# Kernel optimization log

Hardware: AMD Instinct MI355X
Metric: run time of the kernel (lower is better)

The kernel has to match this reference:

```python
import jax, jax.numpy as jnp
import numpy as np

DIM = 1024
HEADS = 16
HEAD_DIM = DIM // HEADS
FFN = 4096
EPS = 1e-6


def layernorm(x, a, b):
    # torch: mean, std (unbiased, ddof=1), divide by (std + eps)
    mean = jnp.mean(x, axis=-1, keepdims=True)
    std = jnp.std(x, axis=-1, keepdims=True, ddof=1)
    return a * (x - mean) / (std + EPS) + b


def setup_inputs() -> dict:
    key = jax.random.key(0)
    ks = jax.random.split(key, 8)
    B, S = 2, 2048
    x = jax.random.normal(ks[0], (B, S, DIM), dtype=jnp.float32)
    mask = jnp.zeros((1, 1, S, S), dtype=jnp.float32)
    sc = 0.02
    wq = jax.random.normal(ks[1], (DIM, DIM), jnp.float32) * sc
    wk = jax.random.normal(ks[2], (DIM, DIM), jnp.float32) * sc
    wv = jax.random.normal(ks[3], (DIM, DIM), jnp.float32) * sc
    wo = jax.random.normal(ks[4], (DIM, DIM), jnp.float32) * sc
    w1 = jax.random.normal(ks[5], (FFN, DIM), jnp.float32) * sc
    w2 = jax.random.normal(ks[6], (DIM, FFN), jnp.float32) * sc
    a1 = jnp.ones((DIM,), jnp.float32)
    b1 = jnp.zeros((DIM,), jnp.float32)
    a2 = jnp.ones((DIM,), jnp.float32)
    b2 = jnp.zeros((DIM,), jnp.float32)
    return {"x": x, "mask": mask, "wq": wq, "wk": wk, "wv": wv, "wo": wo,
            "w1": w1, "w2": w2, "a1": a1, "b1": b1, "a2": a2, "b2": b2}


def reference(x, mask, wq, wk, wv, wo, w1, w2, a1, b1, a2, b2):
    B, S, _ = x.shape
    # QKV projections (Linear weight is [out, in]; y = x @ W.T)
    q = (x @ wq.T).reshape(B, S, HEADS, HEAD_DIM).transpose(0, 2, 1, 3)
    k = (x @ wk.T).reshape(B, S, HEADS, HEAD_DIM).transpose(0, 2, 1, 3)
    v = (x @ wv.T).reshape(B, S, HEADS, HEAD_DIM).transpose(0, 2, 1, 3)
    scores = jnp.einsum('bhqd,bhkd->bhqk', q, k) / np.sqrt(HEAD_DIM).astype(np.float32)
    scores = scores + mask
    probs = jax.nn.softmax(scores.astype(jnp.float32), axis=-1).astype(q.dtype)
    attn = jnp.einsum('bhqk,bhkd->bhqd', probs, v)
    attn = attn.transpose(0, 2, 1, 3).reshape(B, S, DIM)
    attn_out = attn @ wo.T
    attn_x = layernorm(x + attn_out, a1, b1)
    # FFN with exact (erf) GELU, matching nn.GELU default
    h = jax.nn.gelu(attn_x @ w1.T, approximate=False)
    ffn_out = h @ w2.T
    return layernorm(attn_x + ffn_out, a2, b2)
```

## Files before the change

kernel.cpp:

```cpp
#include <hip/hip_runtime.h>
#include <math.h>

typedef __bf16 bf16x8 __attribute__((ext_vector_type(8)));
typedef float  f32x4  __attribute__((ext_vector_type(4)));
typedef unsigned short us4 __attribute__((ext_vector_type(4)));

__device__ __forceinline__ unsigned short f2bf(float f) {
    union { float f; unsigned int u; } v; v.f = f;
    return (unsigned short)((v.u + 0x7FFFu + ((v.u >> 16) & 1u)) >> 16);
}
__device__ __forceinline__ float bf2f(unsigned short u) {
    union { unsigned int i; float f; } c; c.i = (unsigned)u << 16;
    return c.f;
}
__device__ __forceinline__ unsigned cvt_pk_bf16(float lo, float hi) {
    unsigned r;
    asm("v_cvt_pk_bf16_f32 %0, %1, %2" : "=v"(r) : "v"(lo), "v"(hi));
    return r;
}
__device__ __forceinline__ float exp2_raw(float x) {
    float r;
    asm("v_exp_f32 %0, %1" : "=v"(r) : "v"(x));
    return r;
}
__device__ __forceinline__ void gload_lds16(const unsigned short* g, unsigned short* l) {
    __builtin_amdgcn_global_load_lds((__attribute__((address_space(1))) void*)(g),
                                     (__attribute__((address_space(3))) void*)(l), 16, 0, 0);
}

__global__ __launch_bounds__(256)
void cast_all(const float* __restrict__ x, const float* __restrict__ wq,
              const float* __restrict__ wk, const float* __restrict__ wv,
              const float* __restrict__ wo, const float* __restrict__ w1,
              const float* __restrict__ w2,
              unsigned short* __restrict__ xb, unsigned short* __restrict__ wqkv,
              unsigned short* __restrict__ wob, unsigned short* __restrict__ w1b,
              unsigned short* __restrict__ w2b) {
    const int b = blockIdx.x;
    const float* src; unsigned short* dst; int off;
    if      (b <  4096) { src = x;  dst = xb;             off = b;         }
    else if (b <  5120) { src = wq; dst = wqkv;           off = b - 4096;  }
    else if (b <  6144) { src = wk; dst = wqkv + 1048576; off = b - 5120;  }
    else if (b <  7168) { src = wv; dst = wqkv + 2097152; off = b - 6144;  }
    else if (b <  8192) { src = wo; dst = wob;            off = b - 7168;  }
    else if (b < 12288) { src = w1; dst = w1b;            off = b - 8192;  }
    else                { src = w2; dst = w2b;            off = b - 12288; }
    const int i = off * 1024 + threadIdx.x * 4;
    const float4 v = *reinterpret_cast<const float4*>(src + i);
    us4 o = { f2bf(v.x), f2bf(v.y), f2bf(v.z), f2bf(v.w) };
    *reinterpret_cast<us4*>(dst + i) = o;
}

template<int NBI, int EPI>
__global__ __launch_bounds__(512, 2)
void gemm256(const unsigned short* __restrict__ A, const unsigned short* __restrict__ B,
             void* __restrict__ Cout, int M, int N, int Kstride, int Kc, int NBY) {
    constexpr int BN = NBI * 128;
    constexpr int NI = NBI * 2;
    __shared__ __align__(16) unsigned short Al[3][256 * 32];
    __shared__ __align__(16) unsigned short Bl[3][BN * 32];
    const int tid = threadIdx.x;
    const int l   = tid & 63;
    const int w   = tid >> 6;
    const int wg  = blockIdx.x;
    const int swz = (wg & 7) * (gridDim.x >> 3) + (wg >> 3);
    const int bm  = (swz / NBY) * 256;
    const int bn  = (swz % NBY) * BN;
    const int kbase = blockIdx.y * Kc;
    const int wr  = w >> 2;
    const int wc  = w & 3;
    const int wbase = tid & ~63;

    f32x4 acc[8][NI] = {};

    auto stage = [&](int buf, int kt) {
        const int k0 = kbase + kt * 32;
#pragma unroll
        for (int i = 0; i < 2; ++i) {
            const int ci = i * 512 + tid;
            const int r  = ci >> 2;
            const int cl = (ci & 3) ^ (r & 3) ^ ((r >> 2) & 1);
            gload_lds16(A + (size_t)(bm + r) * Kstride + k0 + cl * 8,
                        &Al[buf][(i * 512 + wbase) * 8]);
        }
#pragma unroll
        for (int i = 0; i < NBI; ++i) {
            const int ci = i * 512 + tid;
            const int r  = ci >> 2;
            const int cl = (ci & 3) ^ (r & 3) ^ ((r >> 2) & 1);
            gload_lds16(B + (size_t)(bn + r) * Kstride + k0 + cl * 8,
                        &Bl[buf][(i * 512 + wbase) * 8]);
        }
    };

    const int nk = Kc >> 5;
    stage(0, 0);
    stage(1, 1);
    asm volatile("s_waitcnt vmcnt(%0)" :: "n"(2 + NBI) : "memory");
    __builtin_amdgcn_s_barrier();

    for (int kt = 0; kt < nk; ++kt) {
        const int cur = kt % 3;
        if (kt + 2 < nk) stage((kt + 2) % 3, kt + 2);
        bf16x8 af[8], bfr[NI];
#pragma unroll
        for (int mi = 0; mi < 8; ++mi) {
            const int r  = wr * 128 + mi * 16 + (l & 15);
            const int cl = (l >> 4) ^ (r & 3) ^ ((r >> 2) & 1);
            af[mi] = *reinterpret_cast<const bf16x8*>(&Al[cur][r * 32 + cl * 8]);
        }
#pragma unroll
        for (int ni = 0; ni < NI; ++ni) {
            const int r  = wc * (NI * 16) + ni * 16 + (l & 15);
            const int cl = (l >> 4) ^ (r & 3) ^ ((r >> 2) & 1);
            bfr[ni] = *reinterpret_cast<const bf16x8*>(&Bl[cur][r * 32 + cl * 8]);
        }
        __builtin_amdgcn_s_setprio(1);
#pragma unroll
        for (int mi = 0; mi < 8; ++mi)
#pragma unroll
            for (int ni = 0; ni < NI; ++ni)
                acc[mi][ni] = __builtin_amdgcn_mfma_f32_16x16x32_bf16(af[mi], bfr[ni], acc[mi][ni], 0, 0, 0);
        __builtin_amdgcn_s_setprio(0);
        if (kt + 1 < nk) {
            if (kt + 2 < nk) {
                asm volatile("s_waitcnt vmcnt(%0)" :: "n"(2 + NBI) : "memory");
            } else {
                asm volatile("s_waitcnt vmcnt(0)" ::: "memory");
            }
            __builtin_amdgcn_s_barrier();
        }
    }

#pragma unroll
    for (int mi = 0; mi < 8; ++mi) {
#pragma unroll
        for (int ni = 0; ni < NI; ++ni) {
#pragma unroll
            for (int rr = 0; rr < 4; ++rr) {
                const int m = bm + wr * 128 + mi * 16 + ((l >> 4) << 2) + rr;
                const int n = bn + wc * (NI * 16) + ni * 16 + (l & 15);
                const float v = acc[mi][ni][rr];
                if (EPI == 1) {
                    unsigned short* C = (unsigned short*)Cout;
                    const int s  = m & 2047;
                    const int bh = ((m >> 11) << 4) | ((n & 1023) >> 6);
                    const int d  = n & 63;
                    if (n < 1024)
                        C[(size_t)(bh * 2048 + s) * 64 + d] = f2bf(v * 0.18033688011112042f);
                    else if (n < 2048)
                        C[(size_t)4194304 + (size_t)(bh * 2048 + s) * 64 + d] = f2bf(v);
                    else
                        C[(size_t)8388608 + ((size_t)bh * 64 + d) * 2048 + s] = f2bf(v);
                } else if (EPI == 2) {
                    const float gl = 0.5f * v * (1.0f + erff(v * 0.70710678118654752f));
                    ((unsigned short*)Cout)[(size_t)m * N + n] = f2bf(gl);
                } else {
                    ((unsigned short*)Cout)[(size_t)blockIdx.y * M * N + (size_t)m * N + n] = f2bf(v);
                }
            }
        }
    }
}

__global__ __launch_bounds__(512, 4)
void attn_kernel(const unsigned short* __restrict__ Q, const unsigned short* __restrict__ Kb,
                 const unsigned short* __restrict__ Vt, unsigned short* __restrict__ out) {
    __shared__ __align__(16) unsigned short kld[2][64 * 64];
    __shared__ __align__(16) unsigned short vld[2][64 * 64];
    __shared__ __align__(16) unsigned short plds[8][16][72];
    const int tid = threadIdx.x;
    const int l   = tid & 63;
    const int w   = tid >> 6;
    const int g   = l >> 4;
    const int q15 = l & 15;
    const int bh  = blockIdx.x & 31;
    const int qt  = blockIdx.x >> 5;
    const int q0  = qt * 128 + w * 16;
    const size_t base = (size_t)bh * 2048 * 64;

    bf16x8 qa0, qa1;
    {
        const unsigned short* qp = Q + base + (size_t)(q0 + q15) * 64 + g * 8;
        qa0 = *reinterpret_cast<const bf16x8*>(qp);
        qa1 = *reinterpret_cast<const bf16x8*>(qp + 32);
    }

    bf16x8 ones;
    {
        us4 o1 = { 0x3F80, 0x3F80, 0x3F80, 0x3F80 };
        bf16x8 t;
        *reinterpret_cast<us4*>(&t) = o1;
        *(reinterpret_cast<us4*>(&t) + 1) = o1;
        ones = t;
    }

    f32x4 oacc[5] = {};
    float mrun = -1e30f;

    auto stage = [&](int buf, int k0) {
        const int r  = tid >> 3;
        const int cs = (tid & 7) ^ (r & 7);
        gload_lds16(Kb + base + (size_t)(k0 + r) * 64 + cs * 8, &kld[buf][(tid & ~63) * 8]);
        gload_lds16(Vt + base + (size_t)r * 2048 + k0 + cs * 8, &vld[buf][(tid & ~63) * 8]);
    };

    stage(0, 0);
    int cur = 0;
    for (int t = 0; t < 32; ++t) {
        __syncthreads();
        if (t + 1 < 32) stage(cur ^ 1, (t + 1) * 64);

        bf16x8 kf[4][2];
#pragma unroll
        for (int ks = 0; ks < 4; ++ks) {
            const int row = ks * 16 + q15;
            const int sw  = row & 7;
            kf[ks][0] = *reinterpret_cast<const bf16x8*>(&kld[cur][row * 64 + ((g    ) ^ sw) * 8]);
            kf[ks][1] = *reinterpret_cast<const bf16x8*>(&kld[cur][row * 64 + ((4 + g) ^ sw) * 8]);
        }
        f32x4 sac[4];
#pragma unroll
        for (int ks = 0; ks < 4; ++ks) {
            f32x4 z = { 0.f, 0.f, 0.f, 0.f };
            z = __builtin_amdgcn_mfma_f32_16x16x32_bf16(kf[ks][0], qa0, z, 0, 0, 0);
            z = __builtin_amdgcn_mfma_f32_16x16x32_bf16(kf[ks][1], qa1, z, 0, 0, 0);
            sac[ks] = z;
        }

        float tm = fmaxf(fmaxf(sac[0][0], sac[0][1]), fmaxf(sac[0][2], sac[0][3]));
#pragma unroll
        for (int ks = 1; ks < 4; ++ks) {
            const float a = fmaxf(sac[ks][0], sac[ks][1]);
            const float b = fmaxf(sac[ks][2], sac[ks][3]);
            tm = fmaxf(tm, fmaxf(a, b));
        }
        tm = fmaxf(tm, __shfl_xor(tm, 16));
        tm = fmaxf(tm, __shfl_xor(tm, 32));
        const bool skip = __all(tm <= mrun + 8.0f);
        const float mnew = skip ? mrun : fmaxf(mrun, tm);
#pragma unroll
        for (int ks = 0; ks < 4; ++ks) {
            const float p0 = exp2_raw(sac[ks][0] - mnew);
            const float p1 = exp2_raw(sac[ks][1] - mnew);
            const float p2 = exp2_raw(sac[ks][2] - mnew);
            const float p3 = exp2_raw(sac[ks][3] - mnew);
            uint2 pk;
            pk.x = cvt_pk_bf16(p0, p1);
            pk.y = cvt_pk_bf16(p2, p3);
            *reinterpret_cast<uint2*>(&plds[w][q15][ks * 16 + g * 4]) = pk;
        }
        if (!skip) {
            const float sc = exp2_raw(mrun - mnew);
            float scr[4];
#pragma unroll
            for (int r = 0; r < 4; ++r) scr[r] = __shfl(sc, (l & 48) | (g * 4 + r));
#pragma unroll
            for (int j = 0; j < 5; ++j)
#pragma unroll
                for (int r = 0; r < 4; ++r) oacc[j][r] *= scr[r];
            mrun = mnew;
        }

        const bf16x8 pa0 = *reinterpret_cast<const bf16x8*>(&plds[w][q15][g * 8]);
        const bf16x8 pa1 = *reinterpret_cast<const bf16x8*>(&plds[w][q15][32 + g * 8]);
#pragma unroll
        for (int j = 0; j < 4; ++j) {
            const int row = j * 16 + q15;
            const int sw  = row & 7;
            const bf16x8 v0 = *reinterpret_cast<const bf16x8*>(&vld[cur][row * 64 + ((g    ) ^ sw) * 8]);
            const bf16x8 v1 = *reinterpret_cast<const bf16x8*>(&vld[cur][row * 64 + ((4 + g) ^ sw) * 8]);
            oacc[j] = __builtin_amdgcn_mfma_f32_16x16x32_bf16(pa0, v0, oacc[j], 0, 0, 0);
            oacc[j] = __builtin_amdgcn_mfma_f32_16x16x32_bf16(pa1, v1, oacc[j], 0, 0, 0);
        }
        oacc[4] = __builtin_amdgcn_mfma_f32_16x16x32_bf16(pa0, ones, oacc[4], 0, 0, 0);
        oacc[4] = __builtin_amdgcn_mfma_f32_16x16x32_bf16(pa1, ones, oacc[4], 0, 0, 0);
        cur ^= 1;
    }

    const int b = bh >> 4, h = bh & 15;
#pragma unroll
    for (int r = 0; r < 4; ++r) {
        const float inv = 1.f / oacc[4][r];
        const int q = q0 + g * 4 + r;
#pragma unroll
        for (int j = 0; j < 4; ++j)
            out[(size_t)(b * 2048 + q) * 1024 + h * 64 + j * 16 + q15] = f2bf(oacc[j][r] * inv);
    }
}

template<int NP>
__global__ __launch_bounds__(256)
void ln_res(const float* __restrict__ X, const unsigned short* __restrict__ P,
            const float* __restrict__ gamma, const float* __restrict__ beta,
            float* __restrict__ o32, unsigned short* __restrict__ o16) {
    __shared__ float red[4];
    const int t = threadIdx.x;
    const size_t row = blockIdx.x;
    const float4 a = *reinterpret_cast<const float4*>(X + row * 1024 + t * 4);
    float v0 = a.x, v1 = a.y, v2 = a.z, v3 = a.w;
#pragma unroll
    for (int p = 0; p < NP; ++p) {
        const us4 rr = *reinterpret_cast<const us4*>(P + (size_t)p * 4194304 + row * 1024 + t * 4);
        v0 += bf2f(rr.x); v1 += bf2f(rr.y); v2 += bf2f(rr.z); v3 += bf2f(rr.w);
    }
    float s = v0 + v1 + v2 + v3;
#pragma unroll
    for (int o = 1; o < 64; o <<= 1) s += __shfl_xor(s, o);
    if ((t & 63) == 0) red[t >> 6] = s;
    __syncthreads();
    const float mean = (red[0] + red[1] + red[2] + red[3]) * (1.f / 1024.f);
    v0 -= mean; v1 -= mean; v2 -= mean; v3 -= mean;
    float q = v0 * v0 + v1 * v1 + v2 * v2 + v3 * v3;
#pragma unroll
    for (int o = 1; o < 64; o <<= 1) q += __shfl_xor(q, o);
    __syncthreads();
    if ((t & 63) == 0) red[t >> 6] = q;
    __syncthreads();
    const float var = (red[0] + red[1] + red[2] + red[3]) * (1.f / 1023.f);
    const float inv = 1.f / (sqrtf(var) + 1e-6f);
    const float4 g  = *reinterpret_cast<const float4*>(gamma + t * 4);
    const float4 be = *reinterpret_cast<const float4*>(beta + t * 4);
    const float y0 = g.x * v0 * inv + be.x;
    const float y1 = g.y * v1 * inv + be.y;
    const float y2 = g.z * v2 * inv + be.z;
    const float y3 = g.w * v3 * inv + be.w;
    float4 o4; o4.x = y0; o4.y = y1; o4.z = y2; o4.w = y3;
    *reinterpret_cast<float4*>(o32 + row * 1024 + t * 4) = o4;
    if (o16) {
        us4 ob = { f2bf(y0), f2bf(y1), f2bf(y2), f2bf(y3) };
        *reinterpret_cast<us4*>(o16 + row * 1024 + t * 4) = ob;
    }
}

extern "C" void kernel_launch(void* const* d_in, const int* in_sizes, int n_in,
                              void* d_out, int out_size, void* d_ws, size_t ws_size,
                              hipStream_t stream) {
    const float* x  = (const float*)d_in[0];
    const float* wq = (const float*)d_in[2];
    const float* wk = (const float*)d_in[3];
    const float* wv = (const float*)d_in[4];
    const float* wo = (const float*)d_in[5];
    const float* w1 = (const float*)d_in[6];
    const float* w2 = (const float*)d_in[7];
    const float* a1 = (const float*)d_in[8];
    const float* b1 = (const float*)d_in[9];
    const float* a2 = (const float*)d_in[10];
    const float* b2 = (const float*)d_in[11];

    char* ws = (char*)d_ws;
    const size_t MB = 1024 * 1024;
    unsigned short* xb      = (unsigned short*)(ws);
    unsigned short* wqkv    = (unsigned short*)(ws + 8  * MB);
    unsigned short* wob     = (unsigned short*)(ws + 14 * MB);
    unsigned short* hbuf    = (unsigned short*)(ws);
    unsigned short* w1b     = (unsigned short*)(ws + 32 * MB);
    unsigned short* w2b     = (unsigned short*)(ws + 40 * MB);
    unsigned short* qkv     = (unsigned short*)(ws + 48 * MB);
    unsigned short* projp   = (unsigned short*)(ws + 48 * MB);
    unsigned short* ffn2p   = (unsigned short*)(ws + 48 * MB);
    unsigned short* attn    = (unsigned short*)(ws + 80 * MB);
    float*          attn_x  = (float*)(ws + 88 * MB);
    unsigned short* attn_xb = (unsigned short*)(ws + 104 * MB);

    cast_all<<<16384, 256, 0, stream>>>(x, wq, wk, wv, wo, w1, w2, xb, wqkv, wob, w1b, w2b);
    gemm256<1, 1><<<dim3(384, 1), 512, 0, stream>>>(xb, wqkv, qkv, 4096, 3072, 1024, 1024, 24);
    attn_kernel<<<512, 512, 0, stream>>>(qkv, qkv + 4194304, qkv + 8388608, attn);
    gemm256<2, 3><<<dim3(64, 4), 512, 0, stream>>>(attn, wob, projp, 4096, 1024, 1024, 256, 4);
    ln_res<4><<<4096, 256, 0, stream>>>(x, projp, a1, b1, attn_x, attn_xb);
    gemm256<2, 2><<<dim3(256, 1), 512, 0, stream>>>(attn_xb, w1b, hbuf, 4096, 4096, 1024, 1024, 16);
    gemm256<2, 3><<<dim3(64, 4), 512, 0, stream>>>(hbuf, w2b, ffn2p, 4096, 1024, 4096, 1024, 4);
    ln_res<4><<<4096, 256, 0, stream>>>(attn_x, ffn2p, a2, b2, (float*)d_out, nullptr);
}
```

Before: 271.9 us.

## Replace triple-buffered K=32 GEMM with double-buffered K=64 two-phase 256x256 GEMM

The GEMM kernel now uses a fixed 256x256 output tile with a K-step of 64, double-buffered in LDS, and runs two MFMA phases per stage. It replaces the earlier triple-buffered K=32 pipeline with variable tile width. The LDS layout uses a new XOR swizzle over 8 chunks, and a single __syncthreads per 64-wide K step replaces the fine-grained vmcnt waits. This halves the barrier count and gives each tile more reuse. The QKV GEMM grid drops to 192 blocks, which leaves fewer blocks than CUs. LDS use also grows to 128KB per block, which may lower occupancy and weaken load/compute overlap.

```diff
diff --git a/kernel.cpp b/kernel.cpp
--- a/kernel.cpp
+++ b/kernel.cpp
@@ -51,95 +51,104 @@
     *reinterpret_cast<us4*>(dst + i) = o;
 }
 
-template<int NBI, int EPI>
+template<int EPI>
 __global__ __launch_bounds__(512, 2)
-void gemm256(const unsigned short* __restrict__ A, const unsigned short* __restrict__ B,
-             void* __restrict__ Cout, int M, int N, int Kstride, int Kc, int NBY) {
-    constexpr int BN = NBI * 128;
-    constexpr int NI = NBI * 2;
-    __shared__ __align__(16) unsigned short Al[3][256 * 32];
-    __shared__ __align__(16) unsigned short Bl[3][BN * 32];
+void gemm2ph(const unsigned short* __restrict__ A, const unsigned short* __restrict__ B,
+             void* __restrict__ Cout, int M, int N, int Ks, int Kc, int NBY) {
+    __shared__ __align__(16) unsigned short Al[2][256 * 64];
+    __shared__ __align__(16) unsigned short Bl[2][256 * 64];
     const int tid = threadIdx.x;
     const int l   = tid & 63;
     const int w   = tid >> 6;
+    const int q15 = l & 15;
+    const int g   = l >> 4;
+    const int wr  = w >> 2;
+    const int wc  = w & 3;
     const int wg  = blockIdx.x;
     const int swz = (wg & 7) * (gridDim.x >> 3) + (wg >> 3);
     const int bm  = (swz / NBY) * 256;
-    const int bn  = (swz % NBY) * BN;
+    const int bn  = (swz % NBY) * 256;
     const int kbase = blockIdx.y * Kc;
-    const int wr  = w >> 2;
-    const int wc  = w & 3;
-    const int wbase = tid & ~63;
-
-    f32x4 acc[8][NI] = {};
-
-    auto stage = [&](int buf, int kt) {
-        const int k0 = kbase + kt * 32;
-#pragma unroll
-        for (int i = 0; i < 2; ++i) {
-            const int ci = i * 512 + tid;
-            const int r  = ci >> 2;
-            const int cl = (ci & 3) ^ (r & 3) ^ ((r >> 2) & 1);
-            gload_lds16(A + (size_t)(bm + r) * Kstride + k0 + cl * 8,
-                        &Al[buf][(i * 512 + wbase) * 8]);
-        }
-#pragma unroll
-        for (int i = 0; i < NBI; ++i) {
-            const int ci = i * 512 + tid;
-            const int r  = ci >> 2;
-            const int cl = (ci & 3) ^ (r & 3) ^ ((r >> 2) & 1);
-            gload_lds16(B + (size_t)(bn + r) * Kstride + k0 + cl * 8,
-                        &Bl[buf][(i * 512 + wbase) * 8]);
-        }
+    const int NT  = Kc >> 6;
+
+    const int gta = wc * 64 + l;
+    const int hb  = wc >> 1;
+    const int gtb = (wr * 2 + (wc & 1)) * 64 + l;
+    const int csa = (gta & 7) ^ ((gta >> 3) & 7);
+    const int csb = (gtb & 7) ^ ((gtb >> 3) & 7);
+    const unsigned short* aS = A + (size_t)(bm + wr * 128 + (gta >> 3)) * Ks + kbase + csa * 8;
+    const unsigned short* bS = B + (size_t)(bn + hb * 128 + (gtb >> 3)) * Ks + kbase + csb * 8;
+    const int adst = wr * 8192 + wc * 512;
+    const int bdst = hb * 8192 + (wr * 2 + (wc & 1)) * 512;
+
+    auto stgA = [&](int buf, int j, int ko) {
+        gload_lds16(aS + (size_t)j * 32 * Ks + ko, &Al[0][0] + buf * 16384 + adst + j * 2048);
     };
-
-    const int nk = Kc >> 5;
-    stage(0, 0);
-    stage(1, 1);
-    asm volatile("s_waitcnt vmcnt(%0)" :: "n"(2 + NBI) : "memory");
-    __builtin_amdgcn_s_barrier();
-
-    for (int kt = 0; kt < nk; ++kt) {
-        const int cur = kt % 3;
-        if (kt + 2 < nk) stage((kt + 2) % 3, kt + 2);
-        bf16x8 af[8], bfr[NI];
-#pragma unroll
-        for (int mi = 0; mi < 8; ++mi) {
-            const int r  = wr * 128 + mi * 16 + (l & 15);
-            const int cl = (l >> 4) ^ (r & 3) ^ ((r >> 2) & 1);
-            af[mi] = *reinterpret_cast<const bf16x8*>(&Al[cur][r * 32 + cl * 8]);
-        }
-#pragma unroll
-        for (int ni = 0; ni < NI; ++ni) {
-            const int r  = wc * (NI * 16) + ni * 16 + (l & 15);
-            const int cl = (l >> 4) ^ (r & 3) ^ ((r >> 2) & 1);
-            bfr[ni] = *reinterpret_cast<const bf16x8*>(&Bl[cur][r * 32 + cl * 8]);
-        }
-        __builtin_amdgcn_s_setprio(1);
-#pragma unroll
-        for (int mi = 0; mi < 8; ++mi)
-#pragma unroll
-            for (int ni = 0; ni < NI; ++ni)
-                acc[mi][ni] = __builtin_amdgcn_mfma_f32_16x16x32_bf16(af[mi], bfr[ni], acc[mi][ni], 0, 0, 0);
-        __builtin_amdgcn_s_setprio(0);
-        if (kt + 1 < nk) {
-            if (kt + 2 < nk) {
-                asm volatile("s_waitcnt vmcnt(%0)" :: "n"(2 + NBI) : "memory");
-            } else {
-                asm volatile("s_waitcnt vmcnt(0)" ::: "memory");
-            }
-            __builtin_amdgcn_s_barrier();
-        }
+    auto stgB = [&](int buf, int j, int ko) {
+        gload_lds16(bS + (size_t)j * 32 * Ks + ko, &Bl[0][0] + buf * 16384 + bdst + j * 2048);
+    };
+
+    const int xk0 = g ^ (q15 & 7);
+    const int xk1 = xk0 ^ 4;
+    const int aRd = (wr * 128 + q15) * 64;
+    const int bRd = (hb * 128 + (wc & 1) * 64 + q15) * 64;
+
+    f32x4 acc[8][4] = {};
+
+#pragma unroll
+    for (int j = 0; j < 4; ++j) { stgA(0, j, 0); stgB(0, j, 0); }
+    __syncthreads();
+
+    for (int T = 0; T < NT; ++T) {
+        const int cur = T & 1, nxt = cur ^ 1;
+        const int ko  = (T + 1) << 6;
+        if (T + 1 < NT) {
+#pragma unroll
+            for (int j = 0; j < 4; ++j) { stgA(nxt, j, ko); stgB(nxt, j, ko); }
+        }
+        {
+            bf16x8 a[8], b[4];
+#pragma unroll
+            for (int mi = 0; mi < 8; ++mi)
+                a[mi] = *reinterpret_cast<const bf16x8*>(&Al[0][0] + cur * 16384 + aRd + mi * 1024 + xk0 * 8);
+#pragma unroll
+            for (int ni = 0; ni < 4; ++ni)
+                b[ni] = *reinterpret_cast<const bf16x8*>(&Bl[0][0] + cur * 16384 + bRd + ni * 1024 + xk0 * 8);
+            __builtin_amdgcn_s_setprio(1);
+#pragma unroll
+            for (int mi = 0; mi < 8; ++mi)
+#pragma unroll
+                for (int ni = 0; ni < 4; ++ni)
+                    acc[mi][ni] = __builtin_amdgcn_mfma_f32_16x16x32_bf16(a[mi], b[ni], acc[mi][ni], 0, 0, 0);
+            __builtin_amdgcn_s_setprio(0);
+        }
+        {
+            bf16x8 a[8], b[4];
+#pragma unroll
+            for (int mi = 0; mi < 8; ++mi)
+                a[mi] = *reinterpret_cast<const bf16x8*>(&Al[0][0] + cur * 16384 + aRd + mi * 1024 + xk1 * 8);
+#pragma unroll
+            for (int ni = 0; ni < 4; ++ni)
+                b[ni] = *reinterpret_cast<const bf16x8*>(&Bl[0][0] + cur * 16384 + bRd + ni * 1024 + xk1 * 8);
+            __builtin_amdgcn_s_setprio(1);
+#pragma unroll
+            for (int mi = 0; mi < 8; ++mi)
+#pragma unroll
+                for (int ni = 0; ni < 4; ++ni)
+                    acc[mi][ni] = __builtin_amdgcn_mfma_f32_16x16x32_bf16(a[mi], b[ni], acc[mi][ni], 0, 0, 0);
+            __builtin_amdgcn_s_setprio(0);
+        }
+        __syncthreads();
     }
 
 #pragma unroll
     for (int mi = 0; mi < 8; ++mi) {
 #pragma unroll
-        for (int ni = 0; ni < NI; ++ni) {
+        for (int ni = 0; ni < 4; ++ni) {
 #pragma unroll
             for (int rr = 0; rr < 4; ++rr) {
-                const int m = bm + wr * 128 + mi * 16 + ((l >> 4) << 2) + rr;
-                const int n = bn + wc * (NI * 16) + ni * 16 + (l & 15);
+                const int m = bm + wr * 128 + mi * 16 + (g << 2) + rr;
+                const int n = bn + wc * 64 + ni * 16 + q15;
                 const float v = acc[mi][ni][rr];
                 if (EPI == 1) {
                     unsigned short* C = (unsigned short*)Cout;
@@ -364,11 +373,11 @@
     unsigned short* attn_xb = (unsigned short*)(ws + 104 * MB);
 
     cast_all<<<16384, 256, 0, stream>>>(x, wq, wk, wv, wo, w1, w2, xb, wqkv, wob, w1b, w2b);
-    gemm256<1, 1><<<dim3(384, 1), 512, 0, stream>>>(xb, wqkv, qkv, 4096, 3072, 1024, 1024, 24);
+    gemm2ph<1><<<dim3(192, 1), 512, 0, stream>>>(xb, wqkv, qkv, 4096, 3072, 1024, 1024, 12);
     attn_kernel<<<512, 512, 0, stream>>>(qkv, qkv + 4194304, qkv + 8388608, attn);
-    gemm256<2, 3><<<dim3(64, 4), 512, 0, stream>>>(attn, wob, projp, 4096, 1024, 1024, 256, 4);
+    gemm2ph<3><<<dim3(64, 4), 512, 0, stream>>>(attn, wob, projp, 4096, 1024, 1024, 256, 4);
     ln_res<4><<<4096, 256, 0, stream>>>(x, projp, a1, b1, attn_x, attn_xb);
-    gemm256<2, 2><<<dim3(256, 1), 512, 0, stream>>>(attn_xb, w1b, hbuf, 4096, 4096, 1024, 1024, 16);
-    gemm256<2, 3><<<dim3(64, 4), 512, 0, stream>>>(hbuf, w2b, ffn2p, 4096, 1024, 4096, 1024, 4);
+    gemm2ph<2><<<dim3(256, 1), 512, 0, stream>>>(attn_xb, w1b, hbuf, 4096, 4096, 1024, 1024, 16);
+    gemm2ph<3><<<dim3(64, 4), 512, 0, stream>>>(hbuf, w2b, ffn2p, 4096, 1024, 4096, 1024, 4);
     ln_res<4><<<4096, 256, 0, stream>>>(attn_x, ffn2p, a2, b2, (float*)d_out, nullptr);
 }
```

New measurement: 266.0 us. -2.2%, faster.
